# Kernel tuning notes

Hardware: AMD Instinct MI355X
Metric: run time of the kernel (lower is better)

Reference implementation:

```python
import jax, jax.numpy as jnp
import numpy as np

N_NODES = 50000
N_EDGES = 800000
D_IN = 64
F1 = 64
F2 = 64
D_HID = 100


def setup_inputs() -> dict:
    key = jax.random.key(0)
    ks = jax.random.split(key, 12)
    x = jax.random.normal(ks[0], (N_NODES, D_IN), dtype=jnp.float32)
    edge_src = jax.random.randint(ks[1], (N_EDGES,), 0, N_NODES, dtype=jnp.int32)
    edge_dst = jax.random.randint(ks[2], (N_EDGES,), 0, N_NODES, dtype=jnp.int32)
    # stands in for pre-normalized GCN adjacency values (D^-1/2 (A+I) D^-1/2)
    edge_weight = jax.random.uniform(ks[3], (N_EDGES,), dtype=jnp.float32)
    def glorot(k, shape):
        lim = np.sqrt(6.0 / (shape[0] + shape[1]))
        return jax.random.uniform(k, shape, jnp.float32, -lim, lim)
    W1 = glorot(ks[4], (D_IN, F1))
    b1 = jnp.zeros((F1,), jnp.float32)
    W2 = glorot(ks[5], (F1, F2))
    b2 = jnp.zeros((F2,), jnp.float32)
    Wd = glorot(ks[6], (F2, D_HID))
    bd = jnp.zeros((D_HID,), jnp.float32)
    Wo = glorot(ks[7], (D_HID, 1))
    bo = jnp.zeros((1,), jnp.float32)
    return {"x": x, "edge_src": edge_src, "edge_dst": edge_dst,
            "edge_weight": edge_weight, "W1": W1, "b1": b1, "W2": W2,
            "b2": b2, "Wd": Wd, "bd": bd, "Wo": Wo, "bo": bo}


def _gcn_conv(x, edge_src, edge_dst, edge_weight, W, b):
    # spektral GCNConv: out = swish(A_norm @ (X @ W) + b)
    h = x @ W                                        # [N, F]
    msg = h[edge_src] * edge_weight[:, None]          # [E, F] gather + scale
    agg = jax.ops.segment_sum(msg, edge_dst, num_segments=N_NODES)  # [N, F]
    return jax.nn.swish(agg + b)


def reference(x, edge_src, edge_dst, edge_weight, W1, b1, W2, b2, Wd, bd, Wo, bo):
    h = _gcn_conv(x, edge_src, edge_dst, edge_weight, W1, b1)
    h = _gcn_conv(h, edge_src, edge_dst, edge_weight, W2, b2)
    h = jax.nn.swish(h @ Wd + bd)                    # Dense(100, swish)
    return jax.nn.sigmoid(h @ Wo + bo)               # Dense(1, sigmoid) -> [N, 1]
```

## Files before the change

kernel.cpp:

```cpp
#include <hip/hip_runtime.h>
#include <hip/hip_fp16.h>

#define N_NODES 50000
#define N_EDGES 800000
#define D 64
#define DHID 100
#define NTILES (N_NODES / 16)
#define NCT 7
#define CAP 64
#define NGROUPS 4
#define NSLICES 780
#define FILL_BLOCKS (NGROUPS * NSLICES)
#define MM_BLOCKS ((NTILES + 3) / 4)
#define DST_PER_GROUP (N_NODES / NGROUPS)
#define FSTRIDE (NSLICES * 256)
#define KMAX 5
#define GA_BLOCKS 1024

typedef unsigned short ushort;
typedef unsigned int uint;
typedef __attribute__((ext_vector_type(8))) short s16x8;
typedef __attribute__((ext_vector_type(4))) float f32x4;

#define MFMA16(A, B, C) __builtin_amdgcn_mfma_f32_16x16x32_bf16((A), (B), (C), 0, 0, 0)

__device__ __forceinline__ float swishf(float x) { return x / (1.0f + __expf(-x)); }

__device__ __forceinline__ ushort f2bf(float f) {
    uint u = __float_as_uint(f);
    uint r = (u + 0x7fffu + ((u >> 16) & 1u)) >> 16;
    return (ushort)r;
}
__device__ __forceinline__ float bf2f(ushort h) { return __uint_as_float((uint)h << 16); }
__device__ __forceinline__ float bf_lo(uint d) { return __uint_as_float(d << 16); }
__device__ __forceinline__ float bf_hi(uint d) { return __uint_as_float(d & 0xffff0000u); }

__device__ __forceinline__ float hwf(uint e) {
    return __half2float(__ushort_as_half((ushort)(e >> 16)));
}

__device__ __forceinline__ void accum8(float* acc, uint4 v, float w) {
    acc[0] = fmaf(w, bf_lo(v.x), acc[0]);
    acc[1] = fmaf(w, bf_hi(v.x), acc[1]);
    acc[2] = fmaf(w, bf_lo(v.y), acc[2]);
    acc[3] = fmaf(w, bf_hi(v.y), acc[3]);
    acc[4] = fmaf(w, bf_lo(v.z), acc[4]);
    acc[5] = fmaf(w, bf_hi(v.z), acc[5]);
    acc[6] = fmaf(w, bf_lo(v.w), acc[6]);
    acc[7] = fmaf(w, bf_hi(v.w), acc[7]);
}

__device__ __forceinline__ void gather_body(const ushort* __restrict__ H,
                                            const uint* __restrict__ bucket,
                                            uint4 eA, uint4 eB, int degv,
                                            int j, int fg, float* acc) {
#pragma unroll
    for (int t = 0; t < 8; ++t) acc[t] = 0.f;
    const int sA = j * 4, sB = 16 + j * 4;
    bool pA = sA < degv, pB = sB < degv;
    uint4 vA0, vA1, vA2, vA3, vB0, vB1, vB2, vB3;
    float wA0 = 0, wA1 = 0, wA2 = 0, wA3 = 0;
    float wB0 = 0, wB1 = 0, wB2 = 0, wB3 = 0;
    if (pA) {
        wA0 = hwf(eA.x);
        wA1 = (sA + 1 < degv) ? hwf(eA.y) : 0.f;
        wA2 = (sA + 2 < degv) ? hwf(eA.z) : 0.f;
        wA3 = (sA + 3 < degv) ? hwf(eA.w) : 0.f;
        uint i0 = min(eA.x & 0xffffu, (uint)(N_NODES - 1));
        uint i1 = min(eA.y & 0xffffu, (uint)(N_NODES - 1));
        uint i2 = min(eA.z & 0xffffu, (uint)(N_NODES - 1));
        uint i3 = min(eA.w & 0xffffu, (uint)(N_NODES - 1));
        vA0 = *((const uint4*)(H + ((size_t)i0 << 6) + (fg << 3)));
        vA1 = *((const uint4*)(H + ((size_t)i1 << 6) + (fg << 3)));
        vA2 = *((const uint4*)(H + ((size_t)i2 << 6) + (fg << 3)));
        vA3 = *((const uint4*)(H + ((size_t)i3 << 6) + (fg << 3)));
    }
    if (pB) {
        wB0 = hwf(eB.x);
        wB1 = (sB + 1 < degv) ? hwf(eB.y) : 0.f;
        wB2 = (sB + 2 < degv) ? hwf(eB.z) : 0.f;
        wB3 = (sB + 3 < degv) ? hwf(eB.w) : 0.f;
        uint i0 = min(eB.x & 0xffffu, (uint)(N_NODES - 1));
        uint i1 = min(eB.y & 0xffffu, (uint)(N_NODES - 1));
        uint i2 = min(eB.z & 0xffffu, (uint)(N_NODES - 1));
        uint i3 = min(eB.w & 0xffffu, (uint)(N_NODES - 1));
        vB0 = *((const uint4*)(H + ((size_t)i0 << 6) + (fg << 3)));
        vB1 = *((const uint4*)(H + ((size_t)i1 << 6) + (fg << 3)));
        vB2 = *((const uint4*)(H + ((size_t)i2 << 6) + (fg << 3)));
        vB3 = *((const uint4*)(H + ((size_t)i3 << 6) + (fg << 3)));
    }
    if (pA) {
        accum8(acc, vA0, wA0);
        accum8(acc, vA1, wA1);
        accum8(acc, vA2, wA2);
        accum8(acc, vA3, wA3);
    }
    if (pB) {
        accum8(acc, vB0, wB0);
        accum8(acc, vB1, wB1);
        accum8(acc, vB2, wB2);
        accum8(acc, vB3, wB3);
    }
    for (int base = 32; base < degv; base += 16) {
        int s0 = base + j * 4;
        if (s0 < degv) {
            uint4 e = *((const uint4*)(bucket + s0));
            float w0 = hwf(e.x);
            float w1 = (s0 + 1 < degv) ? hwf(e.y) : 0.f;
            float w2 = (s0 + 2 < degv) ? hwf(e.z) : 0.f;
            float w3 = (s0 + 3 < degv) ? hwf(e.w) : 0.f;
            uint s0i = min(e.x & 0xffffu, (uint)(N_NODES - 1));
            uint s1i = min(e.y & 0xffffu, (uint)(N_NODES - 1));
            uint s2i = min(e.z & 0xffffu, (uint)(N_NODES - 1));
            uint s3i = min(e.w & 0xffffu, (uint)(N_NODES - 1));
            uint4 v0 = *((const uint4*)(H + ((size_t)s0i << 6) + (fg << 3)));
            uint4 v1 = *((const uint4*)(H + ((size_t)s1i << 6) + (fg << 3)));
            uint4 v2 = *((const uint4*)(H + ((size_t)s2i << 6) + (fg << 3)));
            uint4 v3 = *((const uint4*)(H + ((size_t)s3i << 6) + (fg << 3)));
            accum8(acc, v0, w0);
            accum8(acc, v1, w1);
            accum8(acc, v2, w2);
            accum8(acc, v3, w3);
        }
    }
#pragma unroll
    for (int t = 0; t < 8; ++t) {
        acc[t] += __shfl_xor(acc[t], 8, 64);
        acc[t] += __shfl_xor(acc[t], 16, 64);
    }
}

__global__ __launch_bounds__(256) void fill_and_l1(const int* __restrict__ src,
                                                   const int* __restrict__ dst,
                                                   const float* __restrict__ w,
                                                   int* __restrict__ deg,
                                                   uint* __restrict__ csr,
                                                   const float* __restrict__ X,
                                                   const float* __restrict__ W,
                                                   const float* __restrict__ W2,
                                                   const float* __restrict__ Wd,
                                                   short* __restrict__ W2T2,
                                                   short* __restrict__ WdT2,
                                                   ushort* __restrict__ H) {
    __shared__ __align__(16) short sBT[2][D][72];
    int tid = threadIdx.x;

    if (blockIdx.x < FILL_BLOCKS) {
        const int g = blockIdx.x & (NGROUPS - 1);
        const int s = blockIdx.x >> 2;
        const int lo = g * DST_PER_GROUP;
        const int e0 = s * 256 + tid;
        int d[KMAX];
        bool mk[KMAX];
#pragma unroll
        for (int k = 0; k < KMAX; ++k) {
            int e = e0 + k * FSTRIDE;
            int dv = (e < N_EDGES) ? dst[e] : -1;
            d[k] = dv;
            mk[k] = ((uint)(dv - lo) < (uint)DST_PER_GROUP);
        }
        float wv5[KMAX];
        int sv5[KMAX];
#pragma unroll
        for (int k = 0; k < KMAX; ++k)
            if (mk[k]) {
                int e = e0 + k * FSTRIDE;
                wv5[k] = __builtin_nontemporal_load(w + e);
                sv5[k] = __builtin_nontemporal_load(src + e);
            }
        int r5[KMAX];
#pragma unroll
        for (int k = 0; k < KMAX; ++k)
            if (mk[k]) r5[k] = atomicAdd(&deg[d[k]], 1);
#pragma unroll
        for (int k = 0; k < KMAX; ++k)
            if (mk[k]) {
                uint hw = (uint)__half_as_ushort(__float2half_rn(wv5[k]));
                uint payload = (uint)sv5[k] | (hw << 16);
                int r = min(r5[k], CAP - 1);
                csr[(d[k] << 6) + r] = payload;
            }
        return;
    }

    if (blockIdx.x >= FILL_BLOCKS + MM_BLOCKS) {
        if (blockIdx.x == FILL_BLOCKS + MM_BLOCKS) {
            for (int idx = tid; idx < D * D; idx += 256) {
                int k = idx >> 6, c = idx & 63;
                float wv = W2[idx];
                ushort hi = f2bf(wv);
                W2T2[(size_t)c * D + k] = (short)hi;
                W2T2[(size_t)(D + c) * D + k] = (short)f2bf(wv - bf2f(hi));
            }
        } else {
            for (int idx = tid; idx < NCT * 16 * D; idx += 256) {
                int jj = idx >> 6, k = idx & 63;
                float wv = (jj < DHID) ? Wd[k * DHID + jj] : 0.f;
                ushort hi = f2bf(wv);
                WdT2[(size_t)jj * D + k] = (short)hi;
                WdT2[(size_t)(NCT * 16 + jj) * D + k] = (short)f2bf(wv - bf2f(hi));
            }
        }
        return;
    }

    for (int idx = tid; idx < D * D; idx += 256) {
        int k = idx >> 6, c = idx & 63;
        float wv = W[idx];
        ushort hi = f2bf(wv);
        sBT[0][c][k] = (short)hi;
        sBT[1][c][k] = (short)f2bf(wv - bf2f(hi));
    }
    __syncthreads();
    int wv_ = tid >> 6, lane = tid & 63, quad = lane >> 4, m = lane & 15;
    int tile = min((blockIdx.x - FILL_BLOCKS) * 4 + wv_, NTILES - 1);
    int node0 = tile * 16;

    f32x4 acc[4] = {{0,0,0,0},{0,0,0,0},{0,0,0,0},{0,0,0,0}};
#pragma unroll
    for (int kt = 0; kt < 2; ++kt) {
        int k0 = kt * 32 + quad * 8;
        const float* xp = X + ((size_t)(node0 + m) << 6) + k0;
        f32x4 xa = __builtin_nontemporal_load((const f32x4*)xp);
        f32x4 xb = __builtin_nontemporal_load((const f32x4*)(xp + 4));
        float xv[8] = {xa[0], xa[1], xa[2], xa[3], xb[0], xb[1], xb[2], xb[3]};
        s16x8 ahi, alo;
#pragma unroll
        for (int jj = 0; jj < 8; ++jj) {
            ushort hi = f2bf(xv[jj]);
            ahi[jj] = (short)hi;
            alo[jj] = (short)f2bf(xv[jj] - bf2f(hi));
        }
#pragma unroll
        for (int ct = 0; ct < 4; ++ct) {
            int n = ct * 16 + m;
            s16x8 bhi = *((const s16x8*)&sBT[0][n][k0]);
            s16x8 blo = *((const s16x8*)&sBT[1][n][k0]);
            acc[ct] = MFMA16(ahi, bhi, acc[ct]);
            acc[ct] = MFMA16(ahi, blo, acc[ct]);
            acc[ct] = MFMA16(alo, bhi, acc[ct]);
        }
    }
    __syncthreads();
    short (*rep)[16][72] = (short(*)[16][72])&sBT[0][0][0];
#pragma unroll
    for (int ct = 0; ct < 4; ++ct)
#pragma unroll
        for (int r = 0; r < 4; ++r)
            rep[wv_][quad * 4 + r][ct * 16 + m] = (short)f2bf(acc[ct][r]);
#pragma unroll
    for (int half = 0; half < 2; ++half) {
        int r = (lane >> 3) + half * 8;
        int c0 = (lane & 7) * 8;
        s16x8 v = *((const s16x8*)&rep[wv_][r][c0]);
        *((s16x8*)(H + ((size_t)(node0 + r) << 6) + c0)) = v;
    }
}

__global__ __launch_bounds__(256) void gather_act(const ushort* __restrict__ H,
                                                  const int* __restrict__ deg,
                                                  const uint* __restrict__ csr,
                                                  const float* __restrict__ bias,
                                                  ushort* __restrict__ actOut) {
    int tid = threadIdx.x;
    int wave = tid >> 6, lane = tid & 63;
    int h = lane >> 5, j = (lane >> 3) & 3, fg = lane & 7;
    const int NPAIRS = N_NODES / 2;
    const int stride = GA_BLOCKS * 4;
    int pair = blockIdx.x * 4 + wave;
    if (pair >= NPAIRS) return;

    int node = pair * 2 + h;
    const uint* bucket = csr + ((size_t)node << 6);
    uint4 eA = *((const uint4*)(bucket + j * 4));
    uint4 eB = *((const uint4*)(bucket + 16 + j * 4));
    int degv = min(deg[node], CAP);

    for (;;) {
        int npair = pair + stride;
        bool more = (npair < NPAIRS);
        int nnode = more ? (npair * 2 + h) : node;
        const uint* nbucket = csr + ((size_t)nnode << 6);
        uint4 neA = *((const uint4*)(nbucket + j * 4));
        uint4 neB = *((const uint4*)(nbucket + 16 + j * 4));
        int ndeg = min(deg[nnode], CAP);

        float acc[8];
        gather_body(H, bucket, eA, eB, degv, j, fg, acc);
        if (j == 0) {
            float4 ba = ((const float4*)bias)[fg * 2];
            float4 bb = ((const float4*)bias)[fg * 2 + 1];
            float r0 = swishf(acc[0] + ba.x);
            float r1 = swishf(acc[1] + ba.y);
            float r2 = swishf(acc[2] + ba.z);
            float r3 = swishf(acc[3] + ba.w);
            float r4 = swishf(acc[4] + bb.x);
            float r5 = swishf(acc[5] + bb.y);
            float r6 = swishf(acc[6] + bb.z);
            float r7 = swishf(acc[7] + bb.w);
            uint4 u;
            u.x = (uint)f2bf(r0) | ((uint)f2bf(r1) << 16);
            u.y = (uint)f2bf(r2) | ((uint)f2bf(r3) << 16);
            u.z = (uint)f2bf(r4) | ((uint)f2bf(r5) << 16);
            u.w = (uint)f2bf(r6) | ((uint)f2bf(r7) << 16);
            *((uint4*)(actOut + ((size_t)node << 6) + (fg << 3))) = u;
        }

        if (!more) break;
        pair = npair; node = nnode; bucket = nbucket;
        eA = neA; eB = neB; degv = ndeg;
    }
}

__global__ __launch_bounds__(256) void gather_tail(const ushort* __restrict__ act1,
                                                   const int* __restrict__ deg,
                                                   const uint* __restrict__ csr,
                                                   const short* __restrict__ W2T2,
                                                   const float* __restrict__ b2,
                                                   const short* __restrict__ WdT2,
                                                   const float* __restrict__ bd,
                                                   const float* __restrict__ Wo,
                                                   const float* __restrict__ bo,
                                                   float* __restrict__ out) {
    __shared__ __align__(16) float sAgg[16][72];
    __shared__ __align__(16) short sAct2[16][72];
    __shared__ float sPart[4][16];
    int tid = threadIdx.x;
    int wv = tid >> 6, lane = tid & 63;
    int h = lane >> 5, j = (lane >> 3) & 3, fg = lane & 7;
    int quad = lane >> 4, m = lane & 15;
    int node0 = blockIdx.x * 16;

    {
        int n0l = wv * 4 + h, n1l = wv * 4 + 2 + h;
        int n0 = node0 + n0l, n1 = node0 + n1l;
        const uint* b0 = csr + ((size_t)n0 << 6);
        const uint* b1 = csr + ((size_t)n1 << 6);
        uint4 eA0 = *((const uint4*)(b0 + j * 4));
        uint4 eB0 = *((const uint4*)(b0 + 16 + j * 4));
        uint4 eA1 = *((const uint4*)(b1 + j * 4));
        uint4 eB1 = *((const uint4*)(b1 + 16 + j * 4));
        int d0 = min(deg[n0], CAP);
        int d1 = min(deg[n1], CAP);

        float acc0[8];
        gather_body(act1, b0, eA0, eB0, d0, j, fg, acc0);
        if (j == 0) {
            float4 u0 = {acc0[0], acc0[1], acc0[2], acc0[3]};
            float4 u1 = {acc0[4], acc0[5], acc0[6], acc0[7]};
            *((float4*)&sAgg[n0l][fg * 8]) = u0;
            *((float4*)&sAgg[n0l][fg * 8 + 4]) = u1;
        }
        float acc1[8];
        gather_body(act1, b1, eA1, eB1, d1, j, fg, acc1);
        if (j == 0) {
            float4 u0 = {acc1[0], acc1[1], acc1[2], acc1[3]};
            float4 u1 = {acc1[4], acc1[5], acc1[6], acc1[7]};
            *((float4*)&sAgg[n1l][fg * 8]) = u0;
            *((float4*)&sAgg[n1l][fg * 8 + 4]) = u1;
        }
    }
    __syncthreads();

    {
        f32x4 acc = {0, 0, 0, 0};
        int n = wv * 16 + m;
#pragma unroll
        for (int kt = 0; kt < 2; ++kt) {
            int k0 = kt * 32 + quad * 8;
            float4 xa = *((const float4*)&sAgg[m][k0]);
            float4 xb = *((const float4*)&sAgg[m][k0 + 4]);
            float xv[8] = {xa.x, xa.y, xa.z, xa.w, xb.x, xb.y, xb.z, xb.w};
            s16x8 ahi, alo;
#pragma unroll
            for (int jj = 0; jj < 8; ++jj) {
                ushort hi = f2bf(xv[jj]);
                ahi[jj] = (short)hi;
                alo[jj] = (short)f2bf(xv[jj] - bf2f(hi));
            }
            s16x8 bhi = *((const s16x8*)(W2T2 + (size_t)n * D + k0));
            s16x8 blo = *((const s16x8*)(W2T2 + (size_t)(D + n) * D + k0));
            acc = MFMA16(ahi, bhi, acc);
            acc = MFMA16(ahi, blo, acc);
            acc = MFMA16(alo, bhi, acc);
        }
        float bv = b2[n];
#pragma unroll
        for (int r = 0; r < 4; ++r)
            sAct2[quad * 4 + r][n] = (short)f2bf(swishf(acc[r] + bv));
    }
    __syncthreads();

    float part[4] = {0, 0, 0, 0};
#pragma unroll
    for (int cc = 0; cc < 2; ++cc) {
        int ct = wv + cc * 4;
        if (ct < NCT) {
            f32x4 acc = {0, 0, 0, 0};
            int n = ct * 16 + m;
#pragma unroll
            for (int kt = 0; kt < 2; ++kt) {
                int k0 = kt * 32 + quad * 8;
                s16x8 a = *((const s16x8*)&sAct2[m][k0]);
                s16x8 bhi = *((const s16x8*)(WdT2 + (size_t)n * D + k0));
                s16x8 blo = *((const s16x8*)(WdT2 + (size_t)(NCT * 16 + n) * D + k0));
                acc = MFMA16(a, bhi, acc);
                acc = MFMA16(a, blo, acc);
            }
            float bdv = (n < DHID) ? bd[n] : 0.f;
            float wov = (n < DHID) ? Wo[n] : 0.f;
#pragma unroll
            for (int r = 0; r < 4; ++r)
                part[r] = fmaf(swishf(acc[r] + bdv), wov, part[r]);
        }
    }
#pragma unroll
    for (int r = 0; r < 4; ++r) {
        part[r] += __shfl_xor(part[r], 1, 64);
        part[r] += __shfl_xor(part[r], 2, 64);
        part[r] += __shfl_xor(part[r], 4, 64);
        part[r] += __shfl_xor(part[r], 8, 64);
    }
    if (m == 0) {
#pragma unroll
        for (int r = 0; r < 4; ++r)
            sPart[wv][quad * 4 + r] = part[r];
    }
    __syncthreads();
    if (tid < 16) {
        float z = sPart[0][tid] + sPart[1][tid] + sPart[2][tid] + sPart[3][tid] + bo[0];
        out[node0 + tid] = 1.f / (1.f + __expf(-z));
    }
}

extern "C" void kernel_launch(void* const* d_in, const int* in_sizes, int n_in,
                              void* d_out, int out_size, void* d_ws, size_t ws_size,
                              hipStream_t stream) {
    const float* x   = (const float*)d_in[0];
    const int* esrc  = (const int*)d_in[1];
    const int* edst  = (const int*)d_in[2];
    const float* ew  = (const float*)d_in[3];
    const float* W1  = (const float*)d_in[4];
    const float* b1  = (const float*)d_in[5];
    const float* W2  = (const float*)d_in[6];
    const float* b2  = (const float*)d_in[7];
    const float* Wd  = (const float*)d_in[8];
    const float* bd  = (const float*)d_in[9];
    const float* Wo  = (const float*)d_in[10];
    const float* bo  = (const float*)d_in[11];
    float* out = (float*)d_out;

    char* ws = (char*)d_ws;
    ushort* H1   = (ushort*)ws;  ws += (size_t)N_NODES * D * sizeof(ushort);
    ushort* act1 = (ushort*)ws;  ws += (size_t)N_NODES * D * sizeof(ushort);
    uint* csr    = (uint*)ws;    ws += (size_t)N_NODES * CAP * sizeof(uint);
    int* deg     = (int*)ws;     ws += (size_t)N_NODES * sizeof(int);
    short* W2T2  = (short*)ws;   ws += (size_t)2 * D * D * sizeof(short);
    short* WdT2  = (short*)ws;   ws += (size_t)2 * NCT * 16 * D * sizeof(short);

    hipMemsetAsync(deg, 0, (size_t)N_NODES * sizeof(int), stream);

    fill_and_l1<<<FILL_BLOCKS + MM_BLOCKS + 2, 256, 0, stream>>>(
        esrc, edst, ew, deg, csr, x, W1, W2, Wd, W2T2, WdT2, H1);

    gather_act<<<GA_BLOCKS, 256, 0, stream>>>(H1, deg, csr, b1, act1);

    gather_tail<<<NTILES, 256, 0, stream>>>(act1, deg, csr, W2T2, b2, WdT2, bd, Wo, bo, out);
}
```

Measured before the change: 185.5 us.

## Halve CSR bucket capacity and route overflow edges to a global spill list

Shrinks each node's fixed-size edge bucket from 64 to 32 slots, which halves the CSR footprint and the bucket stride. Edges beyond the cap go to a global spill list, and every gather thread scans that whole list to pick up its node's extra edges. The tail loop over buckets larger than 32 is removed, and gather_act switches from a persistent prefetching loop to one launch of 8 nodes per block. The risk is that the linear spill scan by every lane is costly if many nodes exceed degree 32, and that any overflow past the spill limit is dropped silently.

```diff
diff --git a/kernel.cpp b/kernel.cpp
--- a/kernel.cpp
+++ b/kernel.cpp
@@ -7,7 +7,8 @@
 #define DHID 100
 #define NTILES (N_NODES / 16)
 #define NCT 7
-#define CAP 64
+#define CAP 32
+#define SPILL_MAX 8192
 #define NGROUPS 4
 #define NSLICES 780
 #define FILL_BLOCKS (NGROUPS * NSLICES)
@@ -15,7 +16,6 @@
 #define DST_PER_GROUP (N_NODES / NGROUPS)
 #define FSTRIDE (NSLICES * 256)
 #define KMAX 5
-#define GA_BLOCKS 1024
 
 typedef unsigned short ushort;
 typedef unsigned int uint;
@@ -51,7 +51,6 @@
 }
 
 __device__ __forceinline__ void gather_body(const ushort* __restrict__ H,
-                                            const uint* __restrict__ bucket,
                                             uint4 eA, uint4 eB, int degv,
                                             int j, int fg, float* acc) {
 #pragma unroll
@@ -101,32 +100,26 @@
         accum8(acc, vB2, wB2);
         accum8(acc, vB3, wB3);
     }
-    for (int base = 32; base < degv; base += 16) {
-        int s0 = base + j * 4;
-        if (s0 < degv) {
-            uint4 e = *((const uint4*)(bucket + s0));
-            float w0 = hwf(e.x);
-            float w1 = (s0 + 1 < degv) ? hwf(e.y) : 0.f;
-            float w2 = (s0 + 2 < degv) ? hwf(e.z) : 0.f;
-            float w3 = (s0 + 3 < degv) ? hwf(e.w) : 0.f;
-            uint s0i = min(e.x & 0xffffu, (uint)(N_NODES - 1));
-            uint s1i = min(e.y & 0xffffu, (uint)(N_NODES - 1));
-            uint s2i = min(e.z & 0xffffu, (uint)(N_NODES - 1));
-            uint s3i = min(e.w & 0xffffu, (uint)(N_NODES - 1));
-            uint4 v0 = *((const uint4*)(H + ((size_t)s0i << 6) + (fg << 3)));
-            uint4 v1 = *((const uint4*)(H + ((size_t)s1i << 6) + (fg << 3)));
-            uint4 v2 = *((const uint4*)(H + ((size_t)s2i << 6) + (fg << 3)));
-            uint4 v3 = *((const uint4*)(H + ((size_t)s3i << 6) + (fg << 3)));
-            accum8(acc, v0, w0);
-            accum8(acc, v1, w1);
-            accum8(acc, v2, w2);
-            accum8(acc, v3, w3);
-        }
-    }
 #pragma unroll
     for (int t = 0; t < 8; ++t) {
         acc[t] += __shfl_xor(acc[t], 8, 64);
         acc[t] += __shfl_xor(acc[t], 16, 64);
+    }
+}
+
+__device__ __forceinline__ void add_spills(const ushort* __restrict__ H,
+                                           const int* __restrict__ spillCnt,
+                                           const uint2* __restrict__ spill,
+                                           int node, int fg, float* acc) {
+    int n = min(*spillCnt, SPILL_MAX);
+    for (int i = 0; i < n; ++i) {
+        uint2 sp = spill[i];
+        if ((int)sp.x == node) {
+            float wv = hwf(sp.y);
+            uint si = min(sp.y & 0xffffu, (uint)(N_NODES - 1));
+            uint4 v = *((const uint4*)(H + ((size_t)si << 6) + (fg << 3)));
+            accum8(acc, v, wv);
+        }
     }
 }
 
@@ -135,6 +128,8 @@
                                                    const float* __restrict__ w,
                                                    int* __restrict__ deg,
                                                    uint* __restrict__ csr,
+                                                   int* __restrict__ spillCnt,
+                                                   uint2* __restrict__ spill,
                                                    const float* __restrict__ X,
                                                    const float* __restrict__ W,
                                                    const float* __restrict__ W2,
@@ -177,8 +172,13 @@
             if (mk[k]) {
                 uint hw = (uint)__half_as_ushort(__float2half_rn(wv5[k]));
                 uint payload = (uint)sv5[k] | (hw << 16);
-                int r = min(r5[k], CAP - 1);
-                csr[(d[k] << 6) + r] = payload;
+                int r = r5[k];
+                if (r < CAP) {
+                    csr[(d[k] << 5) + r] = payload;
+                } else {
+                    int si = atomicAdd(spillCnt, 1);
+                    if (si < SPILL_MAX) spill[si] = make_uint2((uint)d[k], payload);
+                }
             }
         return;
     }
@@ -260,61 +260,47 @@
 __global__ __launch_bounds__(256) void gather_act(const ushort* __restrict__ H,
                                                   const int* __restrict__ deg,
                                                   const uint* __restrict__ csr,
+                                                  const int* __restrict__ spillCnt,
+                                                  const uint2* __restrict__ spill,
                                                   const float* __restrict__ bias,
                                                   ushort* __restrict__ actOut) {
     int tid = threadIdx.x;
     int wave = tid >> 6, lane = tid & 63;
     int h = lane >> 5, j = (lane >> 3) & 3, fg = lane & 7;
-    const int NPAIRS = N_NODES / 2;
-    const int stride = GA_BLOCKS * 4;
-    int pair = blockIdx.x * 4 + wave;
-    if (pair >= NPAIRS) return;
-
-    int node = pair * 2 + h;
-    const uint* bucket = csr + ((size_t)node << 6);
+    int node = blockIdx.x * 8 + wave * 2 + h;
+    const uint* bucket = csr + ((size_t)node << 5);
     uint4 eA = *((const uint4*)(bucket + j * 4));
     uint4 eB = *((const uint4*)(bucket + 16 + j * 4));
     int degv = min(deg[node], CAP);
 
-    for (;;) {
-        int npair = pair + stride;
-        bool more = (npair < NPAIRS);
-        int nnode = more ? (npair * 2 + h) : node;
-        const uint* nbucket = csr + ((size_t)nnode << 6);
-        uint4 neA = *((const uint4*)(nbucket + j * 4));
-        uint4 neB = *((const uint4*)(nbucket + 16 + j * 4));
-        int ndeg = min(deg[nnode], CAP);
-
-        float acc[8];
-        gather_body(H, bucket, eA, eB, degv, j, fg, acc);
-        if (j == 0) {
-            float4 ba = ((const float4*)bias)[fg * 2];
-            float4 bb = ((const float4*)bias)[fg * 2 + 1];
-            float r0 = swishf(acc[0] + ba.x);
-            float r1 = swishf(acc[1] + ba.y);
-            float r2 = swishf(acc[2] + ba.z);
-            float r3 = swishf(acc[3] + ba.w);
-            float r4 = swishf(acc[4] + bb.x);
-            float r5 = swishf(acc[5] + bb.y);
-            float r6 = swishf(acc[6] + bb.z);
-            float r7 = swishf(acc[7] + bb.w);
-            uint4 u;
-            u.x = (uint)f2bf(r0) | ((uint)f2bf(r1) << 16);
-            u.y = (uint)f2bf(r2) | ((uint)f2bf(r3) << 16);
-            u.z = (uint)f2bf(r4) | ((uint)f2bf(r5) << 16);
-            u.w = (uint)f2bf(r6) | ((uint)f2bf(r7) << 16);
-            *((uint4*)(actOut + ((size_t)node << 6) + (fg << 3))) = u;
-        }
-
-        if (!more) break;
-        pair = npair; node = nnode; bucket = nbucket;
-        eA = neA; eB = neB; degv = ndeg;
+    float acc[8];
+    gather_body(H, eA, eB, degv, j, fg, acc);
+    if (j == 0) {
+        add_spills(H, spillCnt, spill, node, fg, acc);
+        float4 ba = ((const float4*)bias)[fg * 2];
+        float4 bb = ((const float4*)bias)[fg * 2 + 1];
+        float r0 = swishf(acc[0] + ba.x);
+        float r1 = swishf(acc[1] + ba.y);
+        float r2 = swishf(acc[2] + ba.z);
+        float r3 = swishf(acc[3] + ba.w);
+        float r4 = swishf(acc[4] + bb.x);
+        float r5 = swishf(acc[5] + bb.y);
+        float r6 = swishf(acc[6] + bb.z);
+        float r7 = swishf(acc[7] + bb.w);
+        uint4 u;
+        u.x = (uint)f2bf(r0) | ((uint)f2bf(r1) << 16);
+        u.y = (uint)f2bf(r2) | ((uint)f2bf(r3) << 16);
+        u.z = (uint)f2bf(r4) | ((uint)f2bf(r5) << 16);
+        u.w = (uint)f2bf(r6) | ((uint)f2bf(r7) << 16);
+        *((uint4*)(actOut + ((size_t)node << 6) + (fg << 3))) = u;
     }
 }
 
 __global__ __launch_bounds__(256) void gather_tail(const ushort* __restrict__ act1,
                                                    const int* __restrict__ deg,
                                                    const uint* __restrict__ csr,
+                                                   const int* __restrict__ spillCnt,
+                                                   const uint2* __restrict__ spill,
                                                    const short* __restrict__ W2T2,
                                                    const float* __restrict__ b2,
                                                    const short* __restrict__ WdT2,
@@ -334,8 +320,8 @@
     {
         int n0l = wv * 4 + h, n1l = wv * 4 + 2 + h;
         int n0 = node0 + n0l, n1 = node0 + n1l;
-        const uint* b0 = csr + ((size_t)n0 << 6);
-        const uint* b1 = csr + ((size_t)n1 << 6);
+        const uint* b0 = csr + ((size_t)n0 << 5);
+        const uint* b1 = csr + ((size_t)n1 << 5);
         uint4 eA0 = *((const uint4*)(b0 + j * 4));
         uint4 eB0 = *((const uint4*)(b0 + 16 + j * 4));
         uint4 eA1 = *((const uint4*)(b1 + j * 4));
@@ -344,16 +330,18 @@
         int d1 = min(deg[n1], CAP);
 
         float acc0[8];
-        gather_body(act1, b0, eA0, eB0, d0, j, fg, acc0);
+        gather_body(act1, eA0, eB0, d0, j, fg, acc0);
         if (j == 0) {
+            add_spills(act1, spillCnt, spill, n0, fg, acc0);
             float4 u0 = {acc0[0], acc0[1], acc0[2], acc0[3]};
             float4 u1 = {acc0[4], acc0[5], acc0[6], acc0[7]};
             *((float4*)&sAgg[n0l][fg * 8]) = u0;
             *((float4*)&sAgg[n0l][fg * 8 + 4]) = u1;
         }
         float acc1[8];
-        gather_body(act1, b1, eA1, eB1, d1, j, fg, acc1);
+        gather_body(act1, eA1, eB1, d1, j, fg, acc1);
         if (j == 0) {
+            add_spills(act1, spillCnt, spill, n1, fg, acc1);
             float4 u0 = {acc1[0], acc1[1], acc1[2], acc1[3]};
             float4 u1 = {acc1[4], acc1[5], acc1[6], acc1[7]};
             *((float4*)&sAgg[n1l][fg * 8]) = u0;
@@ -451,19 +439,24 @@
     float* out = (float*)d_out;
 
     char* ws = (char*)d_ws;
-    ushort* H1   = (ushort*)ws;  ws += (size_t)N_NODES * D * sizeof(ushort);
-    ushort* act1 = (ushort*)ws;  ws += (size_t)N_NODES * D * sizeof(ushort);
-    uint* csr    = (uint*)ws;    ws += (size_t)N_NODES * CAP * sizeof(uint);
-    int* deg     = (int*)ws;     ws += (size_t)N_NODES * sizeof(int);
-    short* W2T2  = (short*)ws;   ws += (size_t)2 * D * D * sizeof(short);
-    short* WdT2  = (short*)ws;   ws += (size_t)2 * NCT * 16 * D * sizeof(short);
-
-    hipMemsetAsync(deg, 0, (size_t)N_NODES * sizeof(int), stream);
+    ushort* H1    = (ushort*)ws; ws += (size_t)N_NODES * D * sizeof(ushort);
+    ushort* act1  = (ushort*)ws; ws += (size_t)N_NODES * D * sizeof(ushort);
+    uint* csr     = (uint*)ws;   ws += (size_t)N_NODES * CAP * sizeof(uint);
+    int* deg      = (int*)ws;    ws += (size_t)N_NODES * sizeof(int);
+    int* spillCnt = (int*)ws;    ws += 4 * sizeof(int);
+    uint2* spill  = (uint2*)ws;  ws += (size_t)SPILL_MAX * sizeof(uint2);
+    short* W2T2   = (short*)ws;  ws += (size_t)2 * D * D * sizeof(short);
+    short* WdT2   = (short*)ws;  ws += (size_t)2 * NCT * 16 * D * sizeof(short);
+
+    const int gBlocks = N_NODES / 8;
+
+    hipMemsetAsync(deg, 0, (size_t)(N_NODES + 4) * sizeof(int), stream);
 
     fill_and_l1<<<FILL_BLOCKS + MM_BLOCKS + 2, 256, 0, stream>>>(
-        esrc, edst, ew, deg, csr, x, W1, W2, Wd, W2T2, WdT2, H1);
-
-    gather_act<<<GA_BLOCKS, 256, 0, stream>>>(H1, deg, csr, b1, act1);
-
-    gather_tail<<<NTILES, 256, 0, stream>>>(act1, deg, csr, W2T2, b2, WdT2, bd, Wo, bo, out);
-}
+        esrc, edst, ew, deg, csr, spillCnt, spill, x, W1, W2, Wd, W2T2, WdT2, H1);
+
+    gather_act<<<gBlocks, 256, 0, stream>>>(H1, deg, csr, spillCnt, spill, b1, act1);
+
+    gather_tail<<<NTILES, 256, 0, stream>>>(act1, deg, csr, spillCnt, spill,
+                                            W2T2, b2, WdT2, bd, Wo, bo, out);
+}
```

After: 179.7 us (median of 2 runs). 1.03x faster.
